# Kernel tuning notes

Hardware: AMD Instinct MI355X
Metric: run time of the kernel (lower is better)

Reference implementation:

```python
import jax, jax.numpy as jnp
import numpy as np

TEMPERATURE = 0.1

def setup_inputs() -> dict:
    key = jax.random.key(0)
    k1, k2 = jax.random.split(key)
    B, D, NUM_CLASSES = 4096, 512, 64
    emb = jax.random.normal(k1, (B, D), dtype=jnp.float32)
    # L2-normalize so sims/temperature stays in a safe range for exp()
    emb = emb / jnp.linalg.norm(emb, axis=1, keepdims=True)
    labels = jax.random.randint(k2, (B,), 0, NUM_CLASSES, dtype=jnp.int64)
    return {"embeddings": emb, "labels": labels}

def reference(embeddings, labels):
    B = embeddings.shape[0]
    # [B, B] similarity matrix, scaled by temperature
    sims = jnp.matmul(embeddings, embeddings.T) / TEMPERATURE
    same = labels[:, None] == labels[None, :]
    eye = jnp.eye(B, dtype=bool)
    pos_mask = (same & ~eye).astype(sims.dtype)   # positives, diagonal excluded
    neg_mask = (~same).astype(sims.dtype)          # negatives
    exp_s = jnp.exp(sims)
    # denominator[i] = sum over negatives of exp_s[i, :]
    denom = jnp.sum(exp_s * neg_mask, axis=1, keepdims=True)  # [B, 1]
    # per positive pair (i, j): -log(exp_s[i,j] / (denom[i] + exp_s[i,j]))
    per_pair = -jnp.log(exp_s / (denom + exp_s))
    loss_sum = jnp.sum(per_pair * pos_mask)
    num_pos = jnp.sum(pos_mask)
    return loss_sum / jnp.maximum(num_pos, 1.0)
```

## Files before the change

### kernel.cpp

```cpp
#include <hip/hip_runtime.h>
#include <hip/hip_bf16.h>

#define B_N 4096
#define D_K 512
#define INV_T 10.0f

#define BM 128
#define CPB 128
#define CS (B_N / CPB)
#define NCG (CPB / 16)
#define SLOTS 16


typedef __attribute__((ext_vector_type(4))) float float4v;

__global__ __launch_bounds__(256) void k0_convert(const float* __restrict__ emb,
                                                  unsigned char* __restrict__ embT8) {
    int tid = blockIdx.x * 256 + threadIdx.x;
    int l16 = tid & 15;
    int kq  = (tid >> 4) & 63;
    int rg  = tid >> 10;
    int row = rg * 16 + l16;
    const float* sp = emb + row * D_K + kq * 8;
    float4 v0 = *(const float4*)(sp);
    float4 v1 = *(const float4*)(sp + 4);
    int lo = __builtin_amdgcn_cvt_pk_fp8_f32(v0.x, v0.y, 0, false);
    lo     = __builtin_amdgcn_cvt_pk_fp8_f32(v0.z, v0.w, lo, true);
    int hi = __builtin_amdgcn_cvt_pk_fp8_f32(v1.x, v1.y, 0, false);
    hi     = __builtin_amdgcn_cvt_pk_fp8_f32(v1.z, v1.w, hi, true);
    int2 o; o.x = lo; o.y = hi;
    *(int2*)(embT8 + ((rg * 64 + kq) * 16 + l16) * 8) = o;
}

__global__ __launch_bounds__(256, 4) void k1_denom(const unsigned char* __restrict__ embT8,
                                                   const int* __restrict__ labels,
                                                   float* __restrict__ denomPart,
                                                   int* __restrict__ posCnt,
                                                   float* __restrict__ posS) {
    __shared__ unsigned char sB[2][8192];
    __shared__ float sPos[BM * SLOTS];
    __shared__ int   sCnt[BM];

    const int tid  = threadIdx.x;
    const int wave = tid >> 6;
    const int lane = tid & 63;
    const int quad = lane >> 4;
    const int l16  = lane & 15;
    const int bx   = blockIdx.x, by = blockIdx.y;
    const int rowBase = bx * BM;

    if (tid < BM) sCnt[tid] = 0;

#define STAGE(buf, g2)                                                              \
    {                                                                               \
        _Pragma("unroll")                                                           \
        for (int p = 0; p < 2; ++p) {                                               \
            const int seg = (p * 4 + wave) * 1024;                                  \
            const unsigned char* gp = embT8 + (g2) * 8192 + seg + lane * 16;        \
            __builtin_amdgcn_global_load_lds(                                       \
                (const __attribute__((address_space(1))) unsigned int*)gp,          \
                (__attribute__((address_space(3))) unsigned int*)(&sB[buf][seg]),   \
                16, 0, 0);                                                          \
        }                                                                           \
    }

    STAGE(0, by * NCG);

    long afrag[2][16];
#pragma unroll
    for (int t = 0; t < 2; ++t) {
        const int g = bx * 8 + wave * 2 + t;
        const unsigned char* ap = embT8 + (g * 1024 + lane) * 8;
#pragma unroll
        for (int kc = 0; kc < 16; ++kc)
            afrag[t][kc] = *(const long*)(ap + kc * 64 * 8);
    }

    int labI[2][4];
#pragma unroll
    for (int t = 0; t < 2; ++t)
#pragma unroll
        for (int r = 0; r < 4; ++r)
            labI[t][r] = labels[rowBase + wave * 32 + t * 16 + quad * 4 + r];

    int labJ[NCG];
#pragma unroll
    for (int cg = 0; cg < NCG; ++cg)
        labJ[cg] = labels[by * CPB + cg * 16 + l16];

    float rowAcc[2][4] = {{0.f,0.f,0.f,0.f},{0.f,0.f,0.f,0.f}};

    for (int cg = 0; cg < NCG; ++cg) {
        __syncthreads();
        if (cg + 1 < NCG) STAGE((cg + 1) & 1, by * NCG + cg + 1);

        const unsigned char* bt = sB[cg & 1];
        float4v acc[2];
        acc[0] = (float4v){0.f, 0.f, 0.f, 0.f};
        acc[1] = (float4v){0.f, 0.f, 0.f, 0.f};
#pragma unroll
        for (int kc = 0; kc < 16; ++kc) {
            long bfrag = *(const long*)(bt + ((kc * 4 + quad) * 16 + l16) * 8);
            acc[0] = __builtin_amdgcn_mfma_f32_16x16x32_fp8_fp8(afrag[0][kc], bfrag, acc[0], 0, 0, 0);
            acc[1] = __builtin_amdgcn_mfma_f32_16x16x32_fp8_fp8(afrag[1][kc], bfrag, acc[1], 0, 0, 0);
        }

        const int col = by * CPB + cg * 16 + l16;
        const int lJ  = labJ[cg];
#pragma unroll
        for (int t = 0; t < 2; ++t) {
#pragma unroll
            for (int r = 0; r < 4; ++r) {
                float s = acc[t][r] * INV_T;
                const int lr = wave * 32 + t * 16 + quad * 4 + r;
                if (lJ != labI[t][r]) {
                    rowAcc[t][r] += __expf(s);
                } else if (col != rowBase + lr) {
                    int idx = atomicAdd(&sCnt[lr], 1);
                    if (idx < SLOTS) sPos[lr * SLOTS + idx] = s;
                }
            }
        }
    }

#pragma unroll
    for (int t = 0; t < 2; ++t)
#pragma unroll
        for (int r = 0; r < 4; ++r) {
            float v = rowAcc[t][r];
            v += __shfl_xor(v, 1);
            v += __shfl_xor(v, 2);
            v += __shfl_xor(v, 4);
            v += __shfl_xor(v, 8);
            if (l16 == 0)
                denomPart[(rowBase + wave * 32 + t * 16 + quad * 4 + r) * CS + by] = v;
        }

    __syncthreads();
    if (tid < BM) {
        const int row = rowBase + tid;
        const int c   = min(sCnt[tid], SLOTS);
        posCnt[row * CS + by] = c;
        for (int m = 0; m < c; ++m)
            posS[(row * CS + by) * SLOTS + m] = sPos[tid * SLOTS + m];
    }
#undef STAGE
}

__global__ __launch_bounds__(256) void k2_pos(const float* __restrict__ denomPart,
                                              const int* __restrict__ posCnt,
                                              const float* __restrict__ posS,
                                              float* __restrict__ termSum,
                                              float* __restrict__ cntF) {
    const int wave = threadIdx.x >> 6;
    const int lane = threadIdx.x & 63;
    const int i    = blockIdx.x * 4 + wave;

    float d = (lane < CS) ? denomPart[i * CS + lane] : 0.0f;
    float c = (lane < CS) ? (float)posCnt[i * CS + lane] : 0.0f;
#pragma unroll
    for (int off = 32; off; off >>= 1) {
        d += __shfl_xor(d, off);
        c += __shfl_xor(c, off);
    }

    float sum = 0.0f;
#pragma unroll
    for (int it = 0; it < (CS * SLOTS) / 64; ++it) {
        int slot = lane + it * 64;
        int b    = slot >> 4;
        int m    = slot & 15;
        int cb   = posCnt[i * CS + b];
        if (m < cb) {
            float s = posS[i * CS * SLOTS + slot];
            sum += __logf(d + __expf(s)) - s;
        }
    }
#pragma unroll
    for (int off = 32; off; off >>= 1) sum += __shfl_xor(sum, off);
    if (lane == 0) { termSum[i] = sum; cntF[i] = c; }
}

__global__ __launch_bounds__(256) void k3_final(const float* __restrict__ termSum,
                                                const float* __restrict__ cntF,
                                                float* __restrict__ out) {
    __shared__ float sL[256], sC[256];
    float ls = 0.0f, cs = 0.0f;
    for (int i = threadIdx.x; i < B_N; i += 256) { ls += termSum[i]; cs += cntF[i]; }
    sL[threadIdx.x] = ls; sC[threadIdx.x] = cs;
    __syncthreads();
    for (int s = 128; s; s >>= 1) {
        if (threadIdx.x < s) {
            sL[threadIdx.x] += sL[threadIdx.x + s];
            sC[threadIdx.x] += sC[threadIdx.x + s];
        }
        __syncthreads();
    }
    if (threadIdx.x == 0) out[0] = sL[0] / fmaxf(sC[0], 1.0f);
}

extern "C" void kernel_launch(void* const* d_in, const int* in_sizes, int n_in,
                              void* d_out, int out_size, void* d_ws, size_t ws_size,
                              hipStream_t stream) {
    const float* emb    = (const float*)d_in[0];
    const int*   labels = (const int*)d_in[1];
    float*       out    = (float*)d_out;

    char* ws = (char*)d_ws;
    float*         termSum   = (float*)(ws);
    float*         cntF      = (float*)(ws + 16384);
    float*         denomPart = (float*)(ws + 32768);
    int*           posCnt    = (int*)(ws + 557056);
    float*         posS      = (float*)(ws + 1081344);
    unsigned char* embT8     = (unsigned char*)(ws + 12582912);

    k0_convert<<<dim3(B_N * D_K / 8 / 256), dim3(256), 0, stream>>>(emb, embT8);

    k1_denom<<<dim3(B_N / BM, CS), dim3(256), 0, stream>>>(embT8, labels, denomPart, posCnt, posS);

    k2_pos<<<dim3(B_N / 4), dim3(256), 0, stream>>>(denomPart, posCnt, posS, termSum, cntF);

    k3_final<<<dim3(1), dim3(256), 0, stream>>>(termSum, cntF, out);
}
```

Measured before the change: 96.02 us.

## Switch FP8 GEMM to 16x16x128 scaled MFMA with matching fragment layout

Replaces the 16 per-chunk 16x16x32 fp8 MFMAs with four gfx950 16x16x128 scaled f8f6f4 MFMAs per column group, using unit scales. The conversion kernel now writes each 32-byte K fragment as contiguous 16-byte pieces so A and B fragments load as int4 vectors. This cuts the MFMA instruction count and uses wider LDS and global loads, in exchange for a new packed layout that must match the operand lane mapping of the larger instruction exactly.

```diff
diff --git a/kernel.cpp b/kernel.cpp
--- a/kernel.cpp
+++ b/kernel.cpp
@@ -12,24 +12,36 @@
 #define SLOTS 16
 
 
+typedef __attribute__((ext_vector_type(8))) int   int8v;
 typedef __attribute__((ext_vector_type(4))) float float4v;
 
 __global__ __launch_bounds__(256) void k0_convert(const float* __restrict__ emb,
                                                   unsigned char* __restrict__ embT8) {
-    int tid = blockIdx.x * 256 + threadIdx.x;
-    int l16 = tid & 15;
-    int kq  = (tid >> 4) & 63;
-    int rg  = tid >> 10;
-    int row = rg * 16 + l16;
-    const float* sp = emb + row * D_K + kq * 8;
+    int tid  = blockIdx.x * 256 + threadIdx.x;
+    int g    = tid >> 9;
+    int rem  = tid & 511;
+    int kb   = rem >> 7;
+    int rem2 = rem & 127;
+    int h    = rem2 >> 6;
+    int lane = rem2 & 63;
+    int quad = lane >> 4, l16 = lane & 15;
+    int row = g * 16 + l16;
+    int k0  = kb * 128 + quad * 32 + h * 16;
+    const float* sp = emb + row * D_K + k0;
     float4 v0 = *(const float4*)(sp);
     float4 v1 = *(const float4*)(sp + 4);
-    int lo = __builtin_amdgcn_cvt_pk_fp8_f32(v0.x, v0.y, 0, false);
-    lo     = __builtin_amdgcn_cvt_pk_fp8_f32(v0.z, v0.w, lo, true);
-    int hi = __builtin_amdgcn_cvt_pk_fp8_f32(v1.x, v1.y, 0, false);
-    hi     = __builtin_amdgcn_cvt_pk_fp8_f32(v1.z, v1.w, hi, true);
-    int2 o; o.x = lo; o.y = hi;
-    *(int2*)(embT8 + ((rg * 64 + kq) * 16 + l16) * 8) = o;
+    float4 v2 = *(const float4*)(sp + 8);
+    float4 v3 = *(const float4*)(sp + 12);
+    int d0 = __builtin_amdgcn_cvt_pk_fp8_f32(v0.x, v0.y, 0, false);
+    d0     = __builtin_amdgcn_cvt_pk_fp8_f32(v0.z, v0.w, d0, true);
+    int d1 = __builtin_amdgcn_cvt_pk_fp8_f32(v1.x, v1.y, 0, false);
+    d1     = __builtin_amdgcn_cvt_pk_fp8_f32(v1.z, v1.w, d1, true);
+    int d2 = __builtin_amdgcn_cvt_pk_fp8_f32(v2.x, v2.y, 0, false);
+    d2     = __builtin_amdgcn_cvt_pk_fp8_f32(v2.z, v2.w, d2, true);
+    int d3 = __builtin_amdgcn_cvt_pk_fp8_f32(v3.x, v3.y, 0, false);
+    d3     = __builtin_amdgcn_cvt_pk_fp8_f32(v3.z, v3.w, d3, true);
+    int4 o; o.x = d0; o.y = d1; o.z = d2; o.w = d3;
+    *(int4*)(embT8 + (size_t)tid * 16) = o;
 }
 
 __global__ __launch_bounds__(256, 4) void k1_denom(const unsigned char* __restrict__ embT8,
@@ -37,7 +49,7 @@
                                                    float* __restrict__ denomPart,
                                                    int* __restrict__ posCnt,
                                                    float* __restrict__ posS) {
-    __shared__ unsigned char sB[2][8192];
+    __shared__ __align__(16) unsigned char sB[2][8192];
     __shared__ float sPos[BM * SLOTS];
     __shared__ int   sCnt[BM];
 
@@ -56,7 +68,7 @@
         _Pragma("unroll")                                                           \
         for (int p = 0; p < 2; ++p) {                                               \
             const int seg = (p * 4 + wave) * 1024;                                  \
-            const unsigned char* gp = embT8 + (g2) * 8192 + seg + lane * 16;        \
+            const unsigned char* gp = embT8 + (size_t)(g2) * 8192 + seg + lane * 16;\
             __builtin_amdgcn_global_load_lds(                                       \
                 (const __attribute__((address_space(1))) unsigned int*)gp,          \
                 (__attribute__((address_space(3))) unsigned int*)(&sB[buf][seg]),   \
@@ -66,14 +78,16 @@
 
     STAGE(0, by * NCG);
 
-    long afrag[2][16];
+    int8v afrag[2][4];
 #pragma unroll
     for (int t = 0; t < 2; ++t) {
-        const int g = bx * 8 + wave * 2 + t;
-        const unsigned char* ap = embT8 + (g * 1024 + lane) * 8;
-#pragma unroll
-        for (int kc = 0; kc < 16; ++kc)
-            afrag[t][kc] = *(const long*)(ap + kc * 64 * 8);
+        const unsigned char* ap = embT8 + (size_t)(bx * 8 + wave * 2 + t) * 8192;
+#pragma unroll
+        for (int kb = 0; kb < 4; ++kb) {
+            int4 lo = *(const int4*)(ap + (kb * 128 + lane) * 16);
+            int4 hi = *(const int4*)(ap + (kb * 128 + 64 + lane) * 16);
+            afrag[t][kb] = (int8v){lo.x, lo.y, lo.z, lo.w, hi.x, hi.y, hi.z, hi.w};
+        }
     }
 
     int labI[2][4];
@@ -99,10 +113,14 @@
         acc[0] = (float4v){0.f, 0.f, 0.f, 0.f};
         acc[1] = (float4v){0.f, 0.f, 0.f, 0.f};
 #pragma unroll
-        for (int kc = 0; kc < 16; ++kc) {
-            long bfrag = *(const long*)(bt + ((kc * 4 + quad) * 16 + l16) * 8);
-            acc[0] = __builtin_amdgcn_mfma_f32_16x16x32_fp8_fp8(afrag[0][kc], bfrag, acc[0], 0, 0, 0);
-            acc[1] = __builtin_amdgcn_mfma_f32_16x16x32_fp8_fp8(afrag[1][kc], bfrag, acc[1], 0, 0, 0);
+        for (int kb = 0; kb < 4; ++kb) {
+            int4 blo = *(const int4*)(bt + kb * 2048 + lane * 16);
+            int4 bhi = *(const int4*)(bt + kb * 2048 + 1024 + lane * 16);
+            int8v bfrag = (int8v){blo.x, blo.y, blo.z, blo.w, bhi.x, bhi.y, bhi.z, bhi.w};
+            acc[0] = __builtin_amdgcn_mfma_scale_f32_16x16x128_f8f6f4(
+                         afrag[0][kb], bfrag, acc[0], 0, 0, 0, 0x7f7f7f7f, 0, 0x7f7f7f7f);
+            acc[1] = __builtin_amdgcn_mfma_scale_f32_16x16x128_f8f6f4(
+                         afrag[1][kb], bfrag, acc[1], 0, 0, 0, 0x7f7f7f7f, 0, 0x7f7f7f7f);
         }
 
         const int col = by * CPB + cg * 16 + l16;
@@ -214,7 +232,7 @@
     float*         posS      = (float*)(ws + 1081344);
     unsigned char* embT8     = (unsigned char*)(ws + 12582912);
 
-    k0_convert<<<dim3(B_N * D_K / 8 / 256), dim3(256), 0, stream>>>(emb, embT8);
+    k0_convert<<<dim3(B_N * D_K / 16 / 256), dim3(256), 0, stream>>>(emb, embT8);
 
     k1_denom<<<dim3(B_N / BM, CS), dim3(256), 0, stream>>>(embT8, labels, denomPart, posCnt, posS);
 
```

Result: slower. 117.1 us (+21.9%).
